# Optimization experiments

Hardware: AMD Instinct MI355X
Metric: run time of the kernel (lower is better)

## Reference

```python
import jax, jax.numpy as jnp
import numpy as np

N, E, G = 20000, 320000, 128
D, H, C, L = 128, 8, 16, 4  # hidden, heads, per-head dim, layers
F_NODE, F_EDGE, T = 9, 3, 10


def _lin_init(key, fan_in, shape):
    return jax.random.normal(key, shape, dtype=jnp.float32) / np.sqrt(fan_in)


def setup_inputs() -> dict:
    key = jax.random.key(0)
    ks = jax.random.split(key, 24)
    inp = {
        "x": jax.random.normal(ks[0], (N, F_NODE), dtype=jnp.float32),
        "edge_index": jax.random.randint(ks[1], (2, E), 0, N),
        "edge_attr": jax.random.normal(ks[2], (E, F_EDGE), dtype=jnp.float32),
        "batch": jnp.sort(jax.random.randint(ks[3], (N,), 0, G)),
        # encoders
        "node_w": _lin_init(ks[4], F_NODE, (F_NODE, D)), "node_b": jnp.zeros((D,), jnp.float32),
        "edge_w": _lin_init(ks[5], F_EDGE, (F_EDGE, D)), "edge_b": jnp.zeros((D,), jnp.float32),
        # per-layer TransformerConv params (stacked over L)
        "Wq": _lin_init(ks[6], D, (L, D, D)), "bq": jnp.zeros((L, D), jnp.float32),
        "Wk": _lin_init(ks[7], D, (L, D, D)), "bk": jnp.zeros((L, D), jnp.float32),
        "Wv": _lin_init(ks[8], D, (L, D, D)), "bv": jnp.zeros((L, D), jnp.float32),
        "We": _lin_init(ks[9], D, (L, D, D)),  # lin_edge (no bias in PyG)
        "Wskip": _lin_init(ks[10], D, (L, D, D)), "bskip": jnp.zeros((L, D), jnp.float32),
        "Wbeta": _lin_init(ks[11], 3 * D, (L, 3 * D)),  # lin_beta (no bias)
        "ln_g": jnp.ones((L, D), jnp.float32), "ln_b": jnp.zeros((L, D), jnp.float32),
        # prediction head
        "h1_w": _lin_init(ks[12], D, (D, D // 2)), "h1_b": jnp.zeros((D // 2,), jnp.float32),
        "h2_w": _lin_init(ks[13], D // 2, (D // 2, T)), "h2_b": jnp.zeros((T,), jnp.float32),
    }
    return inp


def _layer_norm(x, g, b, eps=1e-5):
    mu = jnp.mean(x, -1, keepdims=True)
    var = jnp.mean(jnp.square(x - mu), -1, keepdims=True)
    return (x - mu) * jax.lax.rsqrt(var + eps) * g + b


def _transformer_conv(h, ea, src, dst, Wq, bq, Wk, bk, Wv, bv, We, Wskip, bskip, Wbeta):
    # PyG TransformerConv, concat=True, beta=True, edge_dim=D, eval mode (no dropout)
    q = (h @ Wq + bq)[dst].reshape(E, H, C)           # query at destination i
    k = (h @ Wk + bk)[src].reshape(E, H, C)
    v = (h @ Wv + bv)[src].reshape(E, H, C)
    e = (ea @ We).reshape(E, H, C)
    k = k + e
    alpha = jnp.sum(q * k, -1) / np.sqrt(C)           # [E, H]
    m = jax.ops.segment_max(alpha, dst, num_segments=N)
    alpha = jnp.exp(alpha - m[dst])
    denom = jax.ops.segment_sum(alpha, dst, num_segments=N)
    alpha = alpha / (denom[dst] + 1e-16)
    msg = (v + e) * alpha[..., None]                  # [E, H, C]
    out = jax.ops.segment_sum(msg, dst, num_segments=N).reshape(N, D)
    x_r = h @ Wskip + bskip                           # root/skip transform
    beta = jax.nn.sigmoid(jnp.concatenate([out, x_r, out - x_r], -1) @ Wbeta)  # [N]
    return beta[:, None] * x_r + (1.0 - beta)[:, None] * out


def reference(x, edge_index, edge_attr, batch, node_w, node_b, edge_w, edge_b,
              Wq, bq, Wk, bk, Wv, bv, We, Wskip, bskip, Wbeta, ln_g, ln_b,
              h1_w, h1_b, h2_w, h2_b):
    src, dst = edge_index[0], edge_index[1]
    h = jax.nn.relu(x @ node_w + node_b)              # node encoder + relu
    ea = edge_attr @ edge_w + edge_b                  # edge encoder
    for l in range(L):
        h_res = h
        h = _transformer_conv(h, ea, src, dst, Wq[l], bq[l], Wk[l], bk[l],
                              Wv[l], bv[l], We[l], Wskip[l], bskip[l], Wbeta[l])
        h = _layer_norm(h + h_res, ln_g[l], ln_b[l])
    # global mean pool over graphs
    sums = jax.ops.segment_sum(h, batch, num_segments=G)
    cnt = jax.ops.segment_sum(jnp.ones((N,), h.dtype), batch, num_segments=G)
    pooled = sums / jnp.maximum(cnt, 1.0)[:, None]    # [G, D]
    return jax.nn.relu(pooled @ h1_w + h1_b) @ h2_w + h2_b  # [G, T]
```

## Files before the change

kernel.cpp:

```cpp
#include <hip/hip_runtime.h>
#include <hip/hip_bf16.h>

typedef __hip_bfloat16 bf16;
typedef __attribute__((ext_vector_type(8))) short short8;
typedef __attribute__((ext_vector_type(4))) float f32x4;

#define DEV __device__ __forceinline__

DEV float blo(unsigned u) { return __uint_as_float(u << 16); }
DEV float bhi(unsigned u) { return __uint_as_float(u & 0xffff0000u); }

DEV float waveReduceSum(float v) {
#pragma unroll
    for (int m = 1; m < 64; m <<= 1) v += __shfl_xor(v, m);
    return v;
}

__global__ __launch_bounds__(256) void pack_w_k(
    const float* __restrict__ Wq, const float* __restrict__ Wk,
    const float* __restrict__ Wv, const float* __restrict__ Ws,
    bf16* __restrict__ outp, int L) {
    int t = blockIdx.x * 256 + threadIdx.x;
    if (t >= 4 * L * 16384) return;
    int p = t & 16383;
    int ls = t >> 14;
    int l = ls >> 2, s = ls & 3;
    int j = p & 7, ln = (p >> 3) & 63, kb = (p >> 9) & 3, nb = p >> 11;
    int k = kb * 32 + (ln >> 4) * 8 + j;
    int n = nb * 16 + (ln & 15);
    const float* W = (s == 0) ? Wq : (s == 1) ? Wk : (s == 2) ? Wv : Ws;
    outp[t] = __float2bfloat16(W[(size_t)l * 16384 + k * 128 + n]);
}

__global__ __launch_bounds__(256) void pack_b_k(
    const float* __restrict__ bq, const float* __restrict__ bk,
    const float* __restrict__ bv, const float* __restrict__ bs,
    float* __restrict__ outp, int L) {
    int t = blockIdx.x * 256 + threadIdx.x;
    if (t >= 4 * L * 128) return;
    int d = t & 127;
    int ls = t >> 7;
    int l = ls >> 2, s = ls & 3;
    const float* B = (s == 0) ? bq : (s == 1) ? bk : (s == 2) ? bv : bs;
    outp[t] = B[l * 128 + d];
}

__global__ __launch_bounds__(256) void edge_mats_k(
    const float* __restrict__ edge_w, const float* __restrict__ edge_b,
    const float* __restrict__ We, float* __restrict__ Me, int L) {
    int t = blockIdx.x * 256 + threadIdx.x;
    if (t >= L * 4 * 128) return;
    int n = t & 127, j = (t >> 7) & 3, l = t >> 9;
    const float* W = We + (size_t)l * 16384;
    const float* row = (j < 3) ? (edge_w + j * 128) : edge_b;
    float acc = 0.f;
    for (int d = 0; d < 128; ++d) acc += row[d] * W[d * 128 + n];
    Me[t] = acc;
}

__global__ __launch_bounds__(256) void hist_k(const int* __restrict__ ei,
                                              int* __restrict__ deg, int E) {
    int e = blockIdx.x * 256 + threadIdx.x;
    if (e >= E) return;
    atomicAdd(&deg[ei[E + e]], 1);
}

__global__ __launch_bounds__(1024) void scan_k(const int* __restrict__ deg,
                                               int* __restrict__ off,
                                               int* __restrict__ cursor, int N, int E) {
    __shared__ int part[1024];
    int t = threadIdx.x;
    int chunk = (N + 1023) >> 10;
    int lo = t * chunk, hi = min(lo + chunk, N);
    int s = 0;
    for (int i = lo; i < hi; ++i) s += deg[i];
    part[t] = s;
    __syncthreads();
    for (int d = 1; d < 1024; d <<= 1) {
        int v = (t >= d) ? part[t - d] : 0;
        __syncthreads();
        part[t] += v;
        __syncthreads();
    }
    int base = (t == 0) ? 0 : part[t - 1];
    for (int i = lo; i < hi; ++i) {
        off[i] = base;
        cursor[i] = base;
        base += deg[i];
    }
    if (t == 1023) off[N] = E;
}

__global__ __launch_bounds__(256) void fill_k(const int* __restrict__ ei,
                                              const float* __restrict__ eattr,
                                              int* __restrict__ cursor,
                                              int* __restrict__ el_src,
                                              float4* __restrict__ ea4, int E) {
    int e = blockIdx.x * 256 + threadIdx.x;
    if (e >= E) return;
    int dst = ei[E + e];
    int pos = atomicAdd(&cursor[dst], 1);
    el_src[pos] = ei[e];
    ea4[pos] = make_float4(eattr[e * 3], eattr[e * 3 + 1], eattr[e * 3 + 2], 0.f);
}

__global__ __launch_bounds__(256) void node_enc_k(
    const float* __restrict__ x, const float* __restrict__ w,
    const float* __restrict__ b, float* __restrict__ h,
    bf16* __restrict__ h_bf, int N) {
    int t = blockIdx.x * 256 + threadIdx.x;
    if (t >= N * 128) return;
    int n = t >> 7, d = t & 127;
    float acc = b[d];
#pragma unroll
    for (int i = 0; i < 9; ++i) acc += x[n * 9 + i] * w[i * 128 + d];
    float r = fmaxf(acc, 0.f);
    h[t] = r;
    h_bf[t] = __float2bfloat16(r);
}

__global__ __launch_bounds__(256) void qkvs_k(
    const bf16* __restrict__ A, const bf16* __restrict__ Wp,
    const float* __restrict__ bp,
    bf16* __restrict__ Q, bf16* __restrict__ kvb,
    float* __restrict__ S, int M) {
    int tid = threadIdx.x;
    int l = tid & 63, w = tid >> 6;
    int row0 = blockIdx.x * 64;
    const short* Ab = (const short*)A + (size_t)(row0 + (l & 15)) * 128 + ((l >> 4) * 8);
    short8 a[4][4];
#pragma unroll
    for (int mb = 0; mb < 4; ++mb)
#pragma unroll
        for (int kb = 0; kb < 4; ++kb)
            a[mb][kb] = *(const short8*)(Ab + mb * 16 * 128 + kb * 32);
    int colb = w * 32 + (l & 15);
#pragma unroll
    for (int s = 0; s < 4; ++s) {
        const short* Wb = (const short*)Wp + s * 16384;
        short8 bfr[2][4];
#pragma unroll
        for (int nbi = 0; nbi < 2; ++nbi)
#pragma unroll
            for (int kb = 0; kb < 4; ++kb)
                bfr[nbi][kb] = *(const short8*)(Wb + (size_t)(((w * 2 + nbi) * 4 + kb) * 64 + l) * 8);
        f32x4 acc[4][2] = {};
#pragma unroll
        for (int kb = 0; kb < 4; ++kb)
#pragma unroll
            for (int mb = 0; mb < 4; ++mb)
#pragma unroll
                for (int nbi = 0; nbi < 2; ++nbi)
                    acc[mb][nbi] = __builtin_amdgcn_mfma_f32_16x16x32_bf16(
                        a[mb][kb], bfr[nbi][kb], acc[mb][nbi], 0, 0, 0);
        float bias0 = bp[s * 128 + colb];
        float bias1 = bp[s * 128 + colb + 16];
#pragma unroll
        for (int mb = 0; mb < 4; ++mb) {
            int rbase = row0 + mb * 16 + (l >> 4) * 4;
#pragma unroll
            for (int j = 0; j < 4; ++j) {
                int r = rbase + j;
                if (r >= M) continue;
#pragma unroll
                for (int nbi = 0; nbi < 2; ++nbi) {
                    int c = colb + nbi * 16;
                    float v = acc[mb][nbi][j] + (nbi ? bias1 : bias0);
                    if (s == 0) {
                        Q[(size_t)r * 128 + c] = __float2bfloat16(v);
                    } else if (s == 3) {
                        S[(size_t)r * 128 + c] = v;
                    } else {
                        size_t idx = ((size_t)r * 64 + (c >> 1)) * 4 + (c & 1) + ((s == 2) ? 2 : 0);
                        kvb[idx] = __float2bfloat16(v);
                    }
                }
            }
        }
    }
}

__global__ __launch_bounds__(256) void attn_k(
    const int* __restrict__ off, const int* __restrict__ el_src,
    const float4* __restrict__ ea4, const float* __restrict__ Me,
    const bf16* __restrict__ Q, const bf16* __restrict__ kvb,
    const float* __restrict__ S,
    float* __restrict__ h, bf16* __restrict__ h_bf,
    const float* __restrict__ Wb, const float* __restrict__ lng,
    const float* __restrict__ lnb, int N) {
    int gw = (blockIdx.x * 256 + threadIdx.x) >> 6;
    int l = threadIdx.x & 63;
    int nw = (gridDim.x * 256) >> 6;
    int d0 = 2 * l, d1 = 2 * l + 1;
    float m00 = Me[d0],       m01 = Me[d1];
    float m10 = Me[128 + d0], m11 = Me[128 + d1];
    float m20 = Me[256 + d0], m21 = Me[256 + d1];
    float mb0 = Me[384 + d0], mb1 = Me[384 + d1];
    float wba0 = Wb[d0],       wba1 = Wb[d1];
    float wbb0 = Wb[128 + d0], wbb1 = Wb[128 + d1];
    float wbc0 = Wb[256 + d0], wbc1 = Wb[256 + d1];
    float g0 = lng[d0], g1 = lng[d1];
    float bb0 = lnb[d0], bb1 = lnb[d1];
    const unsigned* Q2 = (const unsigned*)Q;
    const uint2* KV2 = (const uint2*)kvb;
    for (int n = gw; n < N; n += nw) {
        unsigned q2 = Q2[(size_t)n * 64 + l];
        float q0 = blo(q2) * 0.25f, q1 = bhi(q2) * 0.25f;
        float acc0 = 0.f, acc1 = 0.f, den = 0.f;
        int i0 = off[n], i1 = off[n + 1];
        uint2 kv = make_uint2(0, 0);
        float4 ae = make_float4(0, 0, 0, 0);
        if (i0 < i1) {
            int src0 = el_src[i0];
            ae = ea4[i0];
            kv = KV2[(size_t)src0 * 64 + l];
        }
        for (int i = i0; i < i1; ++i) {
            uint2 kvN = make_uint2(0, 0);
            float4 aeN = make_float4(0, 0, 0, 0);
            if (i + 1 < i1) {
                int srcN = el_src[i + 1];
                aeN = ea4[i + 1];
                kvN = KV2[(size_t)srcN * 64 + l];
            }
            float e0 = fmaf(ae.x, m00, fmaf(ae.y, m10, fmaf(ae.z, m20, mb0)));
            float e1 = fmaf(ae.x, m01, fmaf(ae.y, m11, fmaf(ae.z, m21, mb1)));
            float s = q0 * (blo(kv.x) + e0) + q1 * (bhi(kv.x) + e1);
            s += __shfl_xor(s, 1);
            s += __shfl_xor(s, 2);
            s += __shfl_xor(s, 4);
            float p = __expf(s);
            den += p;
            acc0 += (blo(kv.y) + e0) * p;
            acc1 += (bhi(kv.y) + e1) * p;
            kv = kvN;
            ae = aeN;
        }
        float inv = den > 0.f ? 1.f / den : 0.f;
        float o0 = acc0 * inv, o1 = acc1 * inv;
        size_t base = (size_t)n * 128;
        float s0 = S[base + d0], s1 = S[base + d1];
        float part = o0 * wba0 + s0 * wbb0 + (o0 - s0) * wbc0
                   + o1 * wba1 + s1 * wbb1 + (o1 - s1) * wbc1;
        float g = waveReduceSum(part);
        float beta = 1.f / (1.f + __expf(-g));
        float y0 = beta * s0 + (1.f - beta) * o0;
        float y1 = beta * s1 + (1.f - beta) * o1;
        float z0 = y0 + h[base + d0];
        float z1 = y1 + h[base + d1];
        float mean = waveReduceSum(z0 + z1) * (1.f / 128.f);
        float c0 = z0 - mean, c1 = z1 - mean;
        float var = waveReduceSum(c0 * c0 + c1 * c1) * (1.f / 128.f);
        float invs = rsqrtf(var + 1e-5f);
        float r0 = c0 * invs * g0 + bb0;
        float r1 = c1 * invs * g1 + bb1;
        h[base + d0] = r0;
        h[base + d1] = r1;
        h_bf[base + d0] = __float2bfloat16(r0);
        h_bf[base + d1] = __float2bfloat16(r1);
    }
}

__global__ __launch_bounds__(256) void pool_partial_k(
    const float* __restrict__ h, const int* __restrict__ batch,
    float* __restrict__ psum, int N) {
    int d = threadIdx.x & 127;
    int half = threadIdx.x >> 7;
    int n0 = blockIdx.x * 64;
    int n1 = min(n0 + 64, N);
    float acc = 0.f;
    int curg = -1;
    for (int n = n0 + half; n < n1; n += 2) {
        int g = batch[n];
        if (g != curg) {
            if (curg >= 0) atomicAdd(&psum[curg * 128 + d], acc);
            acc = 0.f;
            curg = g;
        }
        acc += h[(size_t)n * 128 + d];
    }
    if (curg >= 0) atomicAdd(&psum[curg * 128 + d], acc);
}

__global__ __launch_bounds__(128) void head2_k(
    const float* __restrict__ psum, const int* __restrict__ batch,
    const float* __restrict__ h1w, const float* __restrict__ h1b,
    const float* __restrict__ h2w, const float* __restrict__ h2b,
    float* __restrict__ out, int N) {
    int g = blockIdx.x;
    int t = threadIdx.x;
    auto lb = [&](int val) {
        int lo = 0, hi = N;
        while (lo < hi) {
            int mid = (lo + hi) >> 1;
            if (batch[mid] < val) lo = mid + 1; else hi = mid;
        }
        return lo;
    };
    int s = lb(g), e = lb(g + 1);
    float cnt = fmaxf((float)(e - s), 1.f);
    __shared__ float pl[128];
    __shared__ float hid[64];
    pl[t] = psum[g * 128 + t] / cnt;
    __syncthreads();
    if (t < 64) {
        float a = h1b[t];
        for (int k = 0; k < 128; ++k) a += pl[k] * h1w[k * 64 + t];
        hid[t] = fmaxf(a, 0.f);
    }
    __syncthreads();
    if (t < 10) {
        float o = h2b[t];
        for (int k = 0; k < 64; ++k) o += hid[k] * h2w[k * 10 + t];
        out[g * 10 + t] = o;
    }
}

extern "C" void kernel_launch(void* const* d_in, const int* in_sizes, int n_in,
                              void* d_out, int out_size, void* d_ws, size_t ws_size,
                              hipStream_t stream) {
    const float* x      = (const float*)d_in[0];
    const int*   ei     = (const int*)d_in[1];
    const float* eattr  = (const float*)d_in[2];
    const int*   batch  = (const int*)d_in[3];
    const float* node_w = (const float*)d_in[4];
    const float* node_b = (const float*)d_in[5];
    const float* edge_w = (const float*)d_in[6];
    const float* edge_b = (const float*)d_in[7];
    const float* Wq     = (const float*)d_in[8];
    const float* bq     = (const float*)d_in[9];
    const float* Wk     = (const float*)d_in[10];
    const float* bk     = (const float*)d_in[11];
    const float* Wv     = (const float*)d_in[12];
    const float* bv     = (const float*)d_in[13];
    const float* We     = (const float*)d_in[14];
    const float* Wskip  = (const float*)d_in[15];
    const float* bskip  = (const float*)d_in[16];
    const float* Wbeta  = (const float*)d_in[17];
    const float* ln_g   = (const float*)d_in[18];
    const float* ln_b   = (const float*)d_in[19];
    const float* h1_w   = (const float*)d_in[20];
    const float* h1_b   = (const float*)d_in[21];
    const float* h2_w   = (const float*)d_in[22];
    const float* h2_b   = (const float*)d_in[23];
    float* out = (float*)d_out;

    const int N = in_sizes[3];
    const int E = in_sizes[2] / 3;
    const int L = in_sizes[8] / 16384;
    const int G = out_size / 10;

    char* wptr = (char*)d_ws;
    auto alloc = [&](size_t bytes) {
        char* p = wptr;
        wptr += (bytes + 255) & ~(size_t)255;
        return p;
    };
    float* h      = (float*)alloc((size_t)(N + 64) * 128 * 4);
    bf16*  h_bf   = (bf16*)alloc((size_t)(N + 64) * 128 * 2);
    bf16*  Qb     = (bf16*)alloc((size_t)(N + 64) * 128 * 2);
    bf16*  kvb    = (bf16*)alloc((size_t)(N + 64) * 256 * 2);
    float* S      = (float*)alloc((size_t)(N + 64) * 128 * 4);
    float4* ea4   = (float4*)alloc((size_t)E * 16);
    bf16*  Wpack  = (bf16*)alloc((size_t)4 * L * 16384 * 2);
    float* bpack  = (float*)alloc((size_t)4 * L * 128 * 4);
    float* Me     = (float*)alloc((size_t)L * 4 * 128 * 4);
    int*   deg    = (int*)alloc((size_t)N * 4);
    int*   off    = (int*)alloc((size_t)(N + 1) * 4);
    int*   cursor = (int*)alloc((size_t)N * 4);
    int*   el_src = (int*)alloc((size_t)E * 4);
    float* psum   = (float*)alloc((size_t)G * 128 * 4);

    dim3 b256(256), b128(128);

    pack_w_k<<<(4 * L * 16384 + 255) / 256, b256, 0, stream>>>(Wq, Wk, Wv, Wskip, Wpack, L);
    pack_b_k<<<(4 * L * 128 + 255) / 256, b256, 0, stream>>>(bq, bk, bv, bskip, bpack, L);
    edge_mats_k<<<(L * 4 * 128 + 255) / 256, b256, 0, stream>>>(edge_w, edge_b, We, Me, L);
    hipMemsetAsync(deg, 0, (size_t)N * 4, stream);
    hist_k<<<(E + 255) / 256, b256, 0, stream>>>(ei, deg, E);
    scan_k<<<1, 1024, 0, stream>>>(deg, off, cursor, N, E);
    fill_k<<<(E + 255) / 256, b256, 0, stream>>>(ei, eattr, cursor, el_src, ea4, E);
    node_enc_k<<<(N * 128 + 255) / 256, b256, 0, stream>>>(x, node_w, node_b, h, h_bf, N);

    int gN = (N + 63) / 64;
    int gAttn = (N + 3) / 4;
    for (int l = 0; l < L; ++l) {
        qkvs_k<<<gN, b256, 0, stream>>>(h_bf, Wpack + (size_t)l * 4 * 16384,
                                        bpack + (size_t)l * 4 * 128, Qb, kvb, S, N);
        attn_k<<<gAttn, b256, 0, stream>>>(off, el_src, ea4, Me + (size_t)l * 512,
                                           Qb, kvb, S, h, h_bf,
                                           Wbeta + (size_t)l * 384,
                                           ln_g + (size_t)l * 128, ln_b + (size_t)l * 128, N);
    }

    hipMemsetAsync(psum, 0, (size_t)G * 128 * 4, stream);
    pool_partial_k<<<gN, b256, 0, stream>>>(h, batch, psum, N);
    head2_k<<<G, b128, 0, stream>>>(psum, batch, h1_w, h1_b, h2_w, h2_b, out, N);
}
```

Before: 418.0 us.

## Process eight edges per wave with factored edge-embedding attention terms

Restructures attention so each wave handles eight edges at once, with one lane per head and edge slot and 16 channels per lane, instead of looping serially over edges with all 64 lanes on one edge. The edge-feature contribution is folded algebraically: q·(Me·ae) is precomputed per node and head by a new qm_k kernel, and the value-side edge term is rebuilt from three weighted sums of edge attributes after aggregation. K and V are stored as contiguous 128-wide rows for vectorized 16-byte loads. This removes the per-edge shuffle reductions and the serial dependency chain, at the cost of an extra kernel launch, higher register use (16 accumulators), cross-slot reductions at the end, and wasted lanes on low-degree nodes.

```diff
diff --git a/kernel.cpp b/kernel.cpp
--- a/kernel.cpp
+++ b/kernel.cpp
@@ -13,6 +13,13 @@
 DEV float waveReduceSum(float v) {
 #pragma unroll
     for (int m = 1; m < 64; m <<= 1) v += __shfl_xor(v, m);
+    return v;
+}
+
+DEV float red8(float v) {
+    v += __shfl_xor(v, 8);
+    v += __shfl_xor(v, 16);
+    v += __shfl_xor(v, 32);
     return v;
 }
 
@@ -122,7 +129,7 @@
 __global__ __launch_bounds__(256) void qkvs_k(
     const bf16* __restrict__ A, const bf16* __restrict__ Wp,
     const float* __restrict__ bp,
-    bf16* __restrict__ Q, bf16* __restrict__ kvb,
+    bf16* __restrict__ Q, bf16* __restrict__ kv,
     float* __restrict__ S, int M) {
     int tid = threadIdx.x;
     int l = tid & 63, w = tid >> 6;
@@ -171,8 +178,7 @@
                     } else if (s == 3) {
                         S[(size_t)r * 128 + c] = v;
                     } else {
-                        size_t idx = ((size_t)r * 64 + (c >> 1)) * 4 + (c & 1) + ((s == 2) ? 2 : 0);
-                        kvb[idx] = __float2bfloat16(v);
+                        kv[(size_t)r * 256 + ((s == 2) ? 128 : 0) + c] = __float2bfloat16(v);
                     }
                 }
             }
@@ -180,64 +186,97 @@
     }
 }
 
+__global__ __launch_bounds__(256) void qm_k(
+    const bf16* __restrict__ Q, const float* __restrict__ Me,
+    float4* __restrict__ qm, int N) {
+    int t = blockIdx.x * 256 + threadIdx.x;
+    if (t >= N * 8) return;
+    int n = t >> 3, hh = t & 7;
+    const unsigned* qr = (const unsigned*)Q + (size_t)n * 64 + hh * 8;
+    unsigned qq[8];
+    *(uint4*)&qq[0] = *(const uint4*)qr;
+    *(uint4*)&qq[4] = *(const uint4*)(qr + 4);
+    float a0 = 0.f, a1 = 0.f, a2 = 0.f, a3 = 0.f;
+#pragma unroll
+    for (int k = 0; k < 8; ++k) {
+        float x0 = blo(qq[k]), x1 = bhi(qq[k]);
+        int d = hh * 16 + 2 * k;
+        a0 += x0 * Me[d]       + x1 * Me[d + 1];
+        a1 += x0 * Me[128 + d] + x1 * Me[128 + d + 1];
+        a2 += x0 * Me[256 + d] + x1 * Me[256 + d + 1];
+        a3 += x0 * Me[384 + d] + x1 * Me[384 + d + 1];
+    }
+    qm[t] = make_float4(a0, a1, a2, a3);
+}
+
 __global__ __launch_bounds__(256) void attn_k(
     const int* __restrict__ off, const int* __restrict__ el_src,
     const float4* __restrict__ ea4, const float* __restrict__ Me,
-    const bf16* __restrict__ Q, const bf16* __restrict__ kvb,
-    const float* __restrict__ S,
+    const float4* __restrict__ qm, const bf16* __restrict__ Q,
+    const bf16* __restrict__ kv, const float* __restrict__ S,
     float* __restrict__ h, bf16* __restrict__ h_bf,
     const float* __restrict__ Wb, const float* __restrict__ lng,
     const float* __restrict__ lnb, int N) {
     int gw = (blockIdx.x * 256 + threadIdx.x) >> 6;
     int l = threadIdx.x & 63;
     int nw = (gridDim.x * 256) >> 6;
-    int d0 = 2 * l, d1 = 2 * l + 1;
-    float m00 = Me[d0],       m01 = Me[d1];
-    float m10 = Me[128 + d0], m11 = Me[128 + d1];
-    float m20 = Me[256 + d0], m21 = Me[256 + d1];
-    float mb0 = Me[384 + d0], mb1 = Me[384 + d1];
+    int hh = l & 7, sl = l >> 3;
+    int d0 = hh * 16 + sl * 2, d1 = d0 + 1;
+    float me00 = Me[d0],       me01 = Me[d1];
+    float me10 = Me[128 + d0], me11 = Me[128 + d1];
+    float me20 = Me[256 + d0], me21 = Me[256 + d1];
+    float me30 = Me[384 + d0], me31 = Me[384 + d1];
     float wba0 = Wb[d0],       wba1 = Wb[d1];
     float wbb0 = Wb[128 + d0], wbb1 = Wb[128 + d1];
     float wbc0 = Wb[256 + d0], wbc1 = Wb[256 + d1];
     float g0 = lng[d0], g1 = lng[d1];
     float bb0 = lnb[d0], bb1 = lnb[d1];
-    const unsigned* Q2 = (const unsigned*)Q;
-    const uint2* KV2 = (const uint2*)kvb;
     for (int n = gw; n < N; n += nw) {
-        unsigned q2 = Q2[(size_t)n * 64 + l];
-        float q0 = blo(q2) * 0.25f, q1 = bhi(q2) * 0.25f;
-        float acc0 = 0.f, acc1 = 0.f, den = 0.f;
+        const unsigned* qr = (const unsigned*)Q + (size_t)n * 64 + hh * 8;
+        unsigned qq[8];
+        *(uint4*)&qq[0] = *(const uint4*)qr;
+        *(uint4*)&qq[4] = *(const uint4*)(qr + 4);
+        float q[16];
+#pragma unroll
+        for (int k = 0; k < 8; ++k) { q[2 * k] = blo(qq[k]); q[2 * k + 1] = bhi(qq[k]); }
+        float4 qmv = qm[(size_t)n * 8 + hh];
+        float acc[16] = {};
+        float S0 = 0.f, S1 = 0.f, S2 = 0.f, den = 0.f;
         int i0 = off[n], i1 = off[n + 1];
-        uint2 kv = make_uint2(0, 0);
-        float4 ae = make_float4(0, 0, 0, 0);
-        if (i0 < i1) {
-            int src0 = el_src[i0];
-            ae = ea4[i0];
-            kv = KV2[(size_t)src0 * 64 + l];
+        int nit = (i1 - i0 + 7) >> 3;
+        for (int it = 0; it < nit; ++it) {
+            int idx = i0 + it * 8 + sl;
+            bool ok = idx < i1;
+            int ci = ok ? idx : (i1 - 1);
+            int src = el_src[ci];
+            float4 ae = ea4[ci];
+            const unsigned* kr = (const unsigned*)kv + (size_t)src * 128 + hh * 8;
+            unsigned kk[8], vv[8];
+            *(uint4*)&kk[0] = *(const uint4*)kr;
+            *(uint4*)&kk[4] = *(const uint4*)(kr + 4);
+            *(uint4*)&vv[0] = *(const uint4*)(kr + 64);
+            *(uint4*)&vv[4] = *(const uint4*)(kr + 68);
+            float sd = fmaf(ae.x, qmv.x, fmaf(ae.y, qmv.y, fmaf(ae.z, qmv.z, qmv.w)));
+#pragma unroll
+            for (int k = 0; k < 8; ++k)
+                sd = fmaf(q[2 * k], blo(kk[k]), fmaf(q[2 * k + 1], bhi(kk[k]), sd));
+            float p = ok ? __expf(sd * 0.25f) : 0.f;
+            den += p;
+            S0 = fmaf(p, ae.x, S0);
+            S1 = fmaf(p, ae.y, S1);
+            S2 = fmaf(p, ae.z, S2);
+#pragma unroll
+            for (int k = 0; k < 8; ++k) {
+                acc[2 * k]     = fmaf(p, blo(vv[k]), acc[2 * k]);
+                acc[2 * k + 1] = fmaf(p, bhi(vv[k]), acc[2 * k + 1]);
+            }
         }
-        for (int i = i0; i < i1; ++i) {
-            uint2 kvN = make_uint2(0, 0);
-            float4 aeN = make_float4(0, 0, 0, 0);
-            if (i + 1 < i1) {
-                int srcN = el_src[i + 1];
-                aeN = ea4[i + 1];
-                kvN = KV2[(size_t)srcN * 64 + l];
-            }
-            float e0 = fmaf(ae.x, m00, fmaf(ae.y, m10, fmaf(ae.z, m20, mb0)));
-            float e1 = fmaf(ae.x, m01, fmaf(ae.y, m11, fmaf(ae.z, m21, mb1)));
-            float s = q0 * (blo(kv.x) + e0) + q1 * (bhi(kv.x) + e1);
-            s += __shfl_xor(s, 1);
-            s += __shfl_xor(s, 2);
-            s += __shfl_xor(s, 4);
-            float p = __expf(s);
-            den += p;
-            acc0 += (blo(kv.y) + e0) * p;
-            acc1 += (bhi(kv.y) + e1) * p;
-            kv = kvN;
-            ae = aeN;
-        }
+        den = red8(den); S0 = red8(S0); S1 = red8(S1); S2 = red8(S2);
+#pragma unroll
+        for (int k = 0; k < 16; ++k) acc[k] = red8(acc[k]);
         float inv = den > 0.f ? 1.f / den : 0.f;
-        float o0 = acc0 * inv, o1 = acc1 * inv;
+        float o0 = (acc[sl * 2]     + S0 * me00 + S1 * me10 + S2 * me20 + den * me30) * inv;
+        float o1 = (acc[sl * 2 + 1] + S0 * me01 + S1 * me11 + S2 * me21 + den * me31) * inv;
         size_t base = (size_t)n * 128;
         float s0 = S[base + d0], s1 = S[base + d1];
         float part = o0 * wba0 + s0 * wbb0 + (o0 - s0) * wbc0
@@ -359,8 +398,9 @@
     float* h      = (float*)alloc((size_t)(N + 64) * 128 * 4);
     bf16*  h_bf   = (bf16*)alloc((size_t)(N + 64) * 128 * 2);
     bf16*  Qb     = (bf16*)alloc((size_t)(N + 64) * 128 * 2);
-    bf16*  kvb    = (bf16*)alloc((size_t)(N + 64) * 256 * 2);
+    bf16*  kv     = (bf16*)alloc((size_t)(N + 64) * 256 * 2);
     float* S      = (float*)alloc((size_t)(N + 64) * 128 * 4);
+    float4* qm    = (float4*)alloc((size_t)N * 8 * 16);
     float4* ea4   = (float4*)alloc((size_t)E * 16);
     bf16*  Wpack  = (bf16*)alloc((size_t)4 * L * 16384 * 2);
     float* bpack  = (float*)alloc((size_t)4 * L * 128 * 4);
@@ -384,11 +424,14 @@
 
     int gN = (N + 63) / 64;
     int gAttn = (N + 3) / 4;
+    int gQm = (N * 8 + 255) / 256;
     for (int l = 0; l < L; ++l) {
+        const float* Me_l = Me + (size_t)l * 512;
         qkvs_k<<<gN, b256, 0, stream>>>(h_bf, Wpack + (size_t)l * 4 * 16384,
-                                        bpack + (size_t)l * 4 * 128, Qb, kvb, S, N);
-        attn_k<<<gAttn, b256, 0, stream>>>(off, el_src, ea4, Me + (size_t)l * 512,
-                                           Qb, kvb, S, h, h_bf,
+                                        bpack + (size_t)l * 4 * 128, Qb, kv, S, N);
+        qm_k<<<gQm, b256, 0, stream>>>(Qb, Me_l, qm, N);
+        attn_k<<<gAttn, b256, 0, stream>>>(off, el_src, ea4, Me_l, qm,
+                                           Qb, kv, S, h, h_bf,
                                            Wbeta + (size_t)l * 384,
                                            ln_g + (size_t)l * 128, ln_b + (size_t)l * 128, N);
     }
```

Measured after the change: 378.2 us. -9.5%, faster.
